# Performance work log

Hardware: AMD Instinct MI355X
Metric: run time of the kernel (lower is better)

## Reference

```python
import jax, jax.numpy as jnp
import numpy as np
from jax import lax

B, S, L = 128, 256, 10
WORD, CHAR = 50000, 100
TAGS, START, END = 32, 30, 31
WDIM, CDIM, FILT, H = 100, 30, 30, 100
LSTM_IN = WDIM + FILT  # 130
NEG = -10000.0


def setup_inputs() -> dict:
    key = jax.random.key(0)
    ks = jax.random.split(key, 24)
    sc = 0.1
    word_emb = (jax.random.normal(ks[0], (WORD, WDIM), jnp.float32) * sc).at[0].set(0.0)  # padding_idx=0
    char_emb = (jax.random.normal(ks[1], (CHAR, CDIM), jnp.float32) * sc).at[0].set(0.0)
    conv_w = jax.random.normal(ks[2], (FILT, 1, 3, CDIM), jnp.float32) * sc  # OIHW, kernel (3, char_dim)
    conv_b = jax.random.normal(ks[3], (FILT,), jnp.float32) * sc
    wih_f = jax.random.normal(ks[4], (4 * H, LSTM_IN), jnp.float32) * sc
    whh_f = jax.random.normal(ks[5], (4 * H, H), jnp.float32) * sc
    bih_f = jax.random.normal(ks[6], (4 * H,), jnp.float32) * sc
    bhh_f = jax.random.normal(ks[7], (4 * H,), jnp.float32) * sc
    wih_b = jax.random.normal(ks[8], (4 * H, LSTM_IN), jnp.float32) * sc
    whh_b = jax.random.normal(ks[9], (4 * H, H), jnp.float32) * sc
    bih_b = jax.random.normal(ks[10], (4 * H,), jnp.float32) * sc
    bhh_b = jax.random.normal(ks[11], (4 * H,), jnp.float32) * sc
    proj_w = jax.random.normal(ks[12], (TAGS, 2 * H), jnp.float32) * sc
    proj_b = jax.random.normal(ks[13], (TAGS,), jnp.float32) * sc
    trans = jax.random.normal(ks[14], (TAGS, TAGS), jnp.float32)
    trans = trans.at[:, START].set(NEG).at[END, :].set(NEG)  # CRF.reset_parm
    word_x = jax.random.randint(ks[15], (B, S), 1, WORD, jnp.int32)
    char_x = jax.random.randint(ks[16], (B, S, L), 1, CHAR, jnp.int32)
    y = jax.random.randint(ks[17], (B, S), 0, 30, jnp.int32)  # gold tags exclude start/end
    mask = jnp.ones((B, S), jnp.int32)
    return dict(word_emb=word_emb, char_emb=char_emb, conv_w=conv_w, conv_b=conv_b,
                wih_f=wih_f, whh_f=whh_f, bih_f=bih_f, bhh_f=bhh_f,
                wih_b=wih_b, whh_b=whh_b, bih_b=bih_b, bhh_b=bhh_b,
                proj_w=proj_w, proj_b=proj_b, trans=trans,
                word_x=word_x, char_x=char_x, y=y, mask=mask)


def _lstm_dir(x, wih, whh, bih, bhh, reverse):
    # x: [B, S, D] -> hidden states [B, S, H]; PyTorch gate order i, f, g, o
    b = bih + bhh
    xs = jnp.swapaxes(x, 0, 1)  # [S, B, D]
    if reverse:
        xs = xs[::-1]
    Bv = x.shape[0]
    Hd = whh.shape[1]
    init = (jnp.zeros((Bv, Hd), x.dtype), jnp.zeros((Bv, Hd), x.dtype))
    def step(carry, xt):
        h, c = carry
        g = xt @ wih.T + h @ whh.T + b  # [B, 4H]
        i, f, gg, o = jnp.split(g, 4, axis=-1)
        c = jax.nn.sigmoid(f) * c + jax.nn.sigmoid(i) * jnp.tanh(gg)
        h = jax.nn.sigmoid(o) * jnp.tanh(c)
        return (h, c), h
    _, hs = lax.scan(step, init, xs)
    if reverse:
        hs = hs[::-1]
    return jnp.swapaxes(hs, 0, 1)


def _forward(word_emb, char_emb, conv_w, conv_b, wih_f, whh_f, bih_f, bhh_f,
             wih_b, whh_b, bih_b, bhh_b, proj_w, proj_b, trans,
             word_x, char_x, y, mask):
    # --- CharCNN (dropout = identity in eval) ---
    ce = char_emb[char_x].reshape(B * S, 1, L, CDIM)  # [B*S, 1, L, CDIM]
    fm = lax.conv_general_dilated(ce, conv_w, (1, 1), ((2, 2), (0, 0)),
                                  dimension_numbers=('NCHW', 'OIHW', 'NCHW'))
    fm = fm + conv_b[None, :, None, None]  # [B*S, FILT, L+2, 1]
    char_feat = fm.max(axis=(2, 3)).reshape(B, S, FILT)
    # --- BiLSTM + projection ---
    x = jnp.concatenate([word_emb[word_x], char_feat], axis=-1)  # [B, S, 130]
    h_f = _lstm_dir(x, wih_f, whh_f, bih_f, bhh_f, False)
    h_b = _lstm_dir(x, wih_b, whh_b, bih_b, bhh_b, True)
    emission = jnp.concatenate([h_f, h_b], axis=-1) @ proj_w.T + proj_b  # [B, S, TAGS]
    maskf = mask.astype(emission.dtype)
    # --- CRF gold-path score (vectorized form of compute_y_score) ---
    y_pad = jnp.concatenate([jnp.full((B, 1), START, y.dtype), y], axis=1)  # [B, S+1]
    prev, cur = y_pad[:, :-1], y_pad[:, 1:]
    p = jnp.take_along_axis(emission, cur[..., None].astype(jnp.int32), axis=-1)[..., 0]
    t = trans[prev, cur]
    score_y = ((p + t) * maskf).sum(axis=1) + trans[y[:, -1], END]  # original uses last label unmasked
    # --- CRF partition function (logsumexp scan over time) ---
    la0 = jnp.full((B, TAGS), NEG, emission.dtype).at[:, START].set(0.0)
    def step(la, em_m):
        em, m = em_m  # em: [B, TAGS], m: [B]
        la2 = jax.nn.logsumexp(la[:, :, None] + trans[None, :, :] + em[:, None, :], axis=1)
        m = m[:, None]
        return la2 * m + la * (1.0 - m), None
    la, _ = lax.scan(step, la0, (jnp.swapaxes(emission, 0, 1), maskf.T))
    la = la + trans[:, END][None, :]
    total = jax.nn.logsumexp(la, axis=1, keepdims=True)  # [B, 1]
    # faithful to original: [B] - [B,1] broadcasts to [B,B], then mean
    return -jnp.mean(score_y - total)


def reference(word_emb, char_emb, conv_w, conv_b, wih_f, whh_f, bih_f, bhh_f,
              wih_b, whh_b, bih_b, bhh_b, proj_w, proj_b, trans,
              word_x, char_x, y, mask):
    return _forward(word_emb, char_emb, conv_w, conv_b, wih_f, whh_f, bih_f, bhh_f,
                    wih_b, whh_b, bih_b, bhh_b, proj_w, proj_b, trans,
                    word_x, char_x, y, mask)
```

## Files before the change

kernel.cpp:

```cpp
#include <hip/hip_runtime.h>
#include <hip/hip_fp16.h>
#include <cstdint>
#include <cstddef>

#define BB 128
#define SS 256
#define LL 10
#define NTAGS 32
#define TAG_START 30
#define TAG_END 31
#define WDIM 100
#define CDIM 30
#define NFILT 30
#define HDIM 100
#define KIN 130
#define KPAD 160
#define GDIM 400
#define NROWS 832
#define NEGV -10000.0f
#define CTOK 8

#define NB_CONV (BB * SS / CTOK)
#define NB_WORD (BB * SS * KPAD / 256)
#define NB_WCVT (NROWS * KPAD / 256)
#define NB_PRE  (NB_CONV + NB_WORD + NB_WCVT)

typedef _Float16 h2 __attribute__((ext_vector_type(2)));
typedef _Float16 f16x8 __attribute__((ext_vector_type(8)));
typedef float f32x4 __attribute__((ext_vector_type(4)));

__device__ __forceinline__ float sigm(float x) { return 1.0f / (1.0f + __expf(-x)); }
__device__ __forceinline__ float tanh_fast(float x) { return 2.0f / (1.0f + __expf(-2.0f * x)) - 1.0f; }

__device__ __forceinline__ void barrier_lds_only() {
  asm volatile("s_waitcnt lgkmcnt(0)" ::: "memory");
  __builtin_amdgcn_s_barrier();
  asm volatile("" ::: "memory");
}

__global__ __launch_bounds__(256) void k_pre(
    const float* __restrict__ wemb, const int* __restrict__ wx,
    const float* __restrict__ cemb, const float* __restrict__ convw,
    const float* __restrict__ convb, const int* __restrict__ cx,
    const float* __restrict__ wihF, const float* __restrict__ wihB,
    _Float16* __restrict__ x16, _Float16* __restrict__ w16,
    float* __restrict__ out) {
  int blk = blockIdx.x;
  int tid = threadIdx.x;
  if (blk == 0 && tid == 0) out[0] = 0.f;

  if (blk < NB_CONV) {
    int tok8 = tid >> 5;
    int f = tid & 31;
    int token0 = blk * CTOK;
    __shared__ float e[CTOK][LL * CDIM];
    __shared__ float cw[NFILT * 3 * CDIM];
    __shared__ float cb[NFILT];
    __shared__ int ci[CTOK][LL];
    if (tid < CTOK * LL) {
      int t = tid / LL, l = tid - t * LL;
      ci[t][l] = cx[(token0 + t) * LL + l];
    }
    for (int i = tid; i < NFILT * 3 * CDIM; i += 256) cw[i] = convw[i];
    if (tid < NFILT) cb[tid] = convb[tid];
    __syncthreads();
    for (int i = tid; i < CTOK * LL * CDIM; i += 256) {
      int t = i / (LL * CDIM);
      int r = i - t * (LL * CDIM);
      int l = r / CDIM, c = r - l * CDIM;
      e[t][l * CDIM + c] = cemb[ci[t][l] * CDIM + c];
    }
    __syncthreads();
    if (f < NFILT) {
      float d0[LL], d1[LL], d2[LL];
#pragma unroll
      for (int l = 0; l < LL; l++) { d0[l] = 0.f; d1[l] = 0.f; d2[l] = 0.f; }
      const float* et = &e[tok8][0];
      for (int c = 0; c < CDIM; c++) {
        float w0 = cw[(f * 3 + 0) * CDIM + c];
        float w1 = cw[(f * 3 + 1) * CDIM + c];
        float w2 = cw[(f * 3 + 2) * CDIM + c];
#pragma unroll
        for (int l = 0; l < LL; l++) {
          float ev = et[l * CDIM + c];
          d0[l] += ev * w0; d1[l] += ev * w1; d2[l] += ev * w2;
        }
      }
      float bias = cb[f];
      float m = -3.0e38f;
#pragma unroll
      for (int h = 0; h < LL + 2; h++) {
        float acc = bias;
        int j0 = h - 2, j1 = h - 1, j2 = h;
        if (j0 >= 0 && j0 < LL) acc += d0[j0];
        if (j1 >= 0 && j1 < LL) acc += d1[j1];
        if (j2 >= 0 && j2 < LL) acc += d2[j2];
        m = fmaxf(m, acc);
      }
      x16[(size_t)(token0 + tok8) * KPAD + WDIM + f] = (_Float16)m;
    }
  } else if (blk < NB_CONV + NB_WORD) {
    int idx = (blk - NB_CONV) * 256 + tid;
    int token = idx / KPAD;
    int d = idx - token * KPAD;
    if (d < WDIM) {
      x16[idx] = (_Float16)wemb[(size_t)wx[token] * WDIM + d];
    } else if (d >= KIN) {
      x16[idx] = (_Float16)0.f;
    }
  } else {
    int idx = (blk - NB_CONV - NB_WORD) * 256 + tid;
    int n = idx / KPAD;
    int k = idx - n * KPAD;
    float v = 0.f;
    if (k < KIN && n < 2 * GDIM) {
      v = (n < GDIM) ? wihF[(size_t)n * KIN + k] : wihB[(size_t)(n - GDIM) * KIN + k];
    }
    w16[idx] = (_Float16)v;
  }
}

__global__ __launch_bounds__(256) void k_pregemm(
    const _Float16* __restrict__ x16, const _Float16* __restrict__ w16,
    const float* __restrict__ bihF, const float* __restrict__ bhhF,
    const float* __restrict__ bihB, const float* __restrict__ bhhB,
    _Float16* __restrict__ preF, _Float16* __restrict__ preB) {
  __shared__ __align__(16) _Float16 Asl[64 * 40];
  __shared__ __align__(16) _Float16 Bsl[64 * 40];
  int m0 = blockIdx.x * 64;
  int n0 = blockIdx.y * 64;
  int tid = threadIdx.x;
  int lane = tid & 63, w = tid >> 6;
  int quad = lane >> 4, l15 = lane & 15;

  f32x4 acc[4];
#pragma unroll
  for (int i = 0; i < 4; i++) acc[i] = (f32x4){0.f, 0.f, 0.f, 0.f};

  int r = tid >> 2;
  int kk = (tid & 3) * 8;
  const _Float16* xs = x16 + (size_t)(m0 + r) * KPAD + kk;
  const _Float16* wsrc = w16 + (size_t)(n0 + r) * KPAD + kk;

  for (int kc = 0; kc < 5; kc++) {
    if (kc) __syncthreads();
    *(f16x8*)&Asl[r * 40 + kk] = *(const f16x8*)(xs + kc * 32);
    *(f16x8*)&Bsl[r * 40 + kk] = *(const f16x8*)(wsrc + kc * 32);
    __syncthreads();

    f16x8 bfrag = *(const f16x8*)&Bsl[(w * 16 + l15) * 40 + quad * 8];
#pragma unroll
    for (int mt = 0; mt < 4; mt++) {
      f16x8 afrag = *(const f16x8*)&Asl[(mt * 16 + l15) * 40 + quad * 8];
      acc[mt] = __builtin_amdgcn_mfma_f32_16x16x32_f16(afrag, bfrag, acc[mt], 0, 0, 0);
    }
  }

  int ng = n0 + w * 16 + l15;
  if (ng < 2 * GDIM) {
    int dir = ng >= GDIM;
    int jb = dir ? ng - GDIM : ng;
    _Float16* dst = dir ? preB : preF;
    float bias = (dir ? bihB : bihF)[jb] + (dir ? bhhB : bhhF)[jb];
#pragma unroll
    for (int mt = 0; mt < 4; mt++) {
#pragma unroll
      for (int i = 0; i < 4; i++) {
        int m = m0 + mt * 16 + quad * 4 + i;
        dst[(size_t)m * GDIM + jb] = (_Float16)(acc[mt][i] + bias);
      }
    }
  }
}

__global__ __launch_bounds__(448) void k_lstm(
    const _Float16* __restrict__ preF, const _Float16* __restrict__ preB,
    const float* __restrict__ whhF, const float* __restrict__ whhB,
    _Float16* __restrict__ hbuf) {
  int blk = blockIdx.x;
  int dir = blk >> 7;
  int b = blk & 127;
  const _Float16* pre = dir ? preB : preF;
  const float* whh = dir ? whhB : whhF;
  int tid = threadIdx.x;
  int kg = tid / 112;
  int rg = tid - kg * 112;
  bool act = (kg < 4) && (rg < 100);
  int r0 = act ? rg * 4 : 0;
  int kb = (act ? kg : 0) * 32;

  __half2 wp[4][8];
  {
#pragma unroll
    for (int i = 0; i < 4; i++) {
      const float* wr = whh + (size_t)(r0 + i) * HDIM;
#pragma unroll
      for (int q = 0; q < 8; q++) {
        int k0 = kb + 2 * q;
        float w0 = (k0 < HDIM) ? wr[k0] : 0.f;
        float w1 = (k0 + 1 < HDIM) ? wr[k0 + 1] : 0.f;
        wp[i][q] = __floats2half2_rn(w0, w1);
      }
    }
  }

  __shared__ __align__(16) _Float16 hsh16[2][128];
  __shared__ __align__(16) float gpart[4][GDIM];
  if (tid < 128) { hsh16[0][tid] = (_Float16)0.f; hsh16[1][tid] = (_Float16)0.f; }
  float c = 0.f;

  const _Float16* pbase = pre + ((size_t)b * SS + (dir ? (SS - 1) : 0)) * GDIM + r0;
  const intptr_t pstep = dir ? -(intptr_t)GDIM : (intptr_t)GDIM;
  uint2 p0 = {0, 0}, p1 = {0, 0};
  if (act && kg == 0) {
    p0 = *(const uint2*)pbase;
    p1 = *(const uint2*)(pbase + pstep);
  }
  __syncthreads();

  int cur = 0;
  for (int step = 0; step < SS; step++) {
    uint2 p2 = {0, 0};
    if (act && kg == 0) {
      int tn = (step + 2 < SS) ? (step + 2) : (SS - 1);
      p2 = *(const uint2*)(pbase + (intptr_t)tn * pstep);
    }

    if (act) {
      const uint4* h4 = (const uint4*)&hsh16[cur][kb];
      uint4 hv0 = h4[0], hv1 = h4[1];
      __half2 hp[8];
      hp[0] = __builtin_bit_cast(__half2, hv0.x);
      hp[1] = __builtin_bit_cast(__half2, hv0.y);
      hp[2] = __builtin_bit_cast(__half2, hv0.z);
      hp[3] = __builtin_bit_cast(__half2, hv0.w);
      hp[4] = __builtin_bit_cast(__half2, hv1.x);
      hp[5] = __builtin_bit_cast(__half2, hv1.y);
      hp[6] = __builtin_bit_cast(__half2, hv1.z);
      hp[7] = __builtin_bit_cast(__half2, hv1.w);

      float racc[4];
      __half2 z = __floats2half2_rn(0.f, 0.f);
#pragma unroll
      for (int i = 0; i < 4; i++) {
        __half2 a0 = z, a1 = z;
#pragma unroll
        for (int q = 0; q < 8; q += 2) {
          a0 = __hfma2(wp[i][q], hp[q], a0);
          a1 = __hfma2(wp[i][q + 1], hp[q + 1], a1);
        }
        racc[i] = (__low2float(a0) + __high2float(a0)) +
                  (__low2float(a1) + __high2float(a1));
      }
      if (kg == 0) {
        __half2 pa = __builtin_bit_cast(__half2, p0.x);
        __half2 pbv = __builtin_bit_cast(__half2, p0.y);
        racc[0] += __low2float(pa);
        racc[1] += __high2float(pa);
        racc[2] += __low2float(pbv);
        racc[3] += __high2float(pbv);
      }
      *(f32x4*)&gpart[kg][r0] = (f32x4){racc[0], racc[1], racc[2], racc[3]};
    }
    barrier_lds_only();
    if (tid < HDIM) {
      int j = tid;
      float gi = (gpart[0][j] + gpart[1][j]) + (gpart[2][j] + gpart[3][j]);
      float gf = (gpart[0][j + HDIM] + gpart[1][j + HDIM]) + (gpart[2][j + HDIM] + gpart[3][j + HDIM]);
      float gg = (gpart[0][j + 2 * HDIM] + gpart[1][j + 2 * HDIM]) + (gpart[2][j + 2 * HDIM] + gpart[3][j + 2 * HDIM]);
      float go = (gpart[0][j + 3 * HDIM] + gpart[1][j + 3 * HDIM]) + (gpart[2][j + 3 * HDIM] + gpart[3][j + 3 * HDIM]);
      float ig = sigm(gi), fg = sigm(gf), g2 = tanh_fast(gg), og = sigm(go);
      c = fg * c + ig * g2;
      float h = og * tanh_fast(c);
      hsh16[cur ^ 1][j] = (_Float16)h;
      int t = dir ? (SS - 1 - step) : step;
      hbuf[((size_t)b * SS + t) * (2 * HDIM) + dir * HDIM + j] = (_Float16)h;
    }
    barrier_lds_only();
    p0 = p1; p1 = p2;
    cur ^= 1;
  }
}

__global__ __launch_bounds__(256) void k_proj(const _Float16* __restrict__ hbuf,
                                              const float* __restrict__ pw,
                                              const float* __restrict__ pb,
                                              float* __restrict__ em) {
  __shared__ __align__(16) float pws[NTAGS * 204];
  __shared__ float pbs[NTAGS];
  int tid = threadIdx.x;
  for (int i = tid; i < NTAGS * 2 * HDIM; i += 256) {
    int tag = i / (2 * HDIM);
    int k = i - tag * (2 * HDIM);
    pws[tag * 204 + k] = pw[i];
  }
  if (tid < NTAGS) pbs[tid] = pb[tid];
  __syncthreads();

  int idx = blockIdx.x * blockDim.x + tid;
  if (idx >= BB * SS * NTAGS) return;
  int token = idx >> 5, tag = idx & 31;
  const uint4* h4 = (const uint4*)(hbuf + (size_t)token * 2 * HDIM);
  const float4* w4 = (const float4*)&pws[tag * 204];
  float acc = pbs[tag];
#pragma unroll
  for (int k = 0; k < 25; k++) {
    uint4 hv = h4[k];
    h2 a = __builtin_bit_cast(h2, hv.x);
    h2 bq = __builtin_bit_cast(h2, hv.y);
    h2 cq = __builtin_bit_cast(h2, hv.z);
    h2 d = __builtin_bit_cast(h2, hv.w);
    float4 w0 = w4[k * 2], w1 = w4[k * 2 + 1];
    acc += (float)a.x * w0.x + (float)a.y * w0.y + (float)bq.x * w0.z + (float)bq.y * w0.w
         + (float)cq.x * w1.x + (float)cq.y * w1.y + (float)d.x * w1.z + (float)d.y * w1.w;
  }
  em[idx] = acc;
}

__global__ __launch_bounds__(64) void k_crf(const float* __restrict__ em,
                                            const float* __restrict__ trans,
                                            const int* __restrict__ mask,
                                            const int* __restrict__ y,
                                            float* __restrict__ out) {
  int b = blockIdx.x;
  int lane = threadIdx.x;
  int j = lane & 31;
  int h = lane >> 5;

  float sacc = 0.f;
  for (int s = lane; s < SS; s += 64) {
    int curt = y[b * SS + s];
    int prevt = (s == 0) ? TAG_START : y[b * SS + s - 1];
    float mk = (float)mask[b * SS + s];
    sacc += (em[((size_t)b * SS + s) * NTAGS + curt] + trans[prevt * NTAGS + curt]) * mk;
  }
#pragma unroll
  for (int off = 32; off > 0; off >>= 1) sacc += __shfl_down(sacc, off);
  float scoreYv = __shfl(sacc, 0) + trans[y[b * SS + SS - 1] * NTAGS + TAG_END];

  float tcol[16];
#pragma unroll
  for (int i = 0; i < 16; i++) tcol[i] = trans[(h * 16 + i) * NTAGS + j];

  float la = (j == TAG_START) ? 0.f : NEGV;

  const float* emb = em + (size_t)b * SS * NTAGS + j;
  const int* mkb = mask + b * SS;
  float e0 = emb[0], e1 = emb[NTAGS];
  int m0i = mkb[0], m1i = mkb[1];

  for (int s = 0; s < SS; s++) {
    int sn = (s + 2 < SS) ? (s + 2) : (SS - 1);
    float e2 = emb[(size_t)sn * NTAGS];
    int m2i = mkb[sn];

    float v[16];
#pragma unroll
    for (int i = 0; i < 16; i++) v[i] = __shfl(la, h * 16 + i) + tcol[i];

    float ma = v[0], mb2 = v[1];
#pragma unroll
    for (int i = 2; i < 16; i += 2) { ma = fmaxf(ma, v[i]); mb2 = fmaxf(mb2, v[i + 1]); }
    float mh = fmaxf(ma, mb2);
    float m = fmaxf(mh, __shfl_xor(mh, 32));

    float sa = 0.f, sb = 0.f;
#pragma unroll
    for (int i = 0; i < 16; i += 2) { sa += __expf(v[i] - m); sb += __expf(v[i + 1] - m); }
    float sh = sa + sb;
    float sum = sh + __shfl_xor(sh, 32);

    float la2 = m + __logf(sum) + e0;
    float mk = (float)m0i;
    la = la2 * mk + la * (1.f - mk);
    e0 = e1; e1 = e2; m0i = m1i; m1i = m2i;
  }
  la += trans[j * NTAGS + TAG_END];

  float mm = la;
#pragma unroll
  for (int off = 16; off > 0; off >>= 1) mm = fmaxf(mm, __shfl_xor(mm, off));
  float ss = __expf(la - mm);
#pragma unroll
  for (int off = 16; off > 0; off >>= 1) ss += __shfl_xor(ss, off);
  float total = mm + __logf(ss);
  if (lane == 0) atomicAdd(out, (total - scoreYv) * (1.0f / BB));
}

extern "C" void kernel_launch(void* const* d_in, const int* in_sizes, int n_in,
                              void* d_out, int out_size, void* d_ws, size_t ws_size,
                              hipStream_t stream) {
  const float* word_emb = (const float*)d_in[0];
  const float* char_emb = (const float*)d_in[1];
  const float* conv_w   = (const float*)d_in[2];
  const float* conv_b   = (const float*)d_in[3];
  const float* wih_f    = (const float*)d_in[4];
  const float* whh_f    = (const float*)d_in[5];
  const float* bih_f    = (const float*)d_in[6];
  const float* bhh_f    = (const float*)d_in[7];
  const float* wih_b    = (const float*)d_in[8];
  const float* whh_b    = (const float*)d_in[9];
  const float* bih_b    = (const float*)d_in[10];
  const float* bhh_b    = (const float*)d_in[11];
  const float* proj_w   = (const float*)d_in[12];
  const float* proj_b   = (const float*)d_in[13];
  const float* trans    = (const float*)d_in[14];
  const int* word_x     = (const int*)d_in[15];
  const int* char_x     = (const int*)d_in[16];
  const int* y          = (const int*)d_in[17];
  const int* mask       = (const int*)d_in[18];
  float* out = (float*)d_out;

  _Float16* x16   = (_Float16*)d_ws;
  _Float16* w16   = x16 + (size_t)BB * SS * KPAD;
  _Float16* preF  = w16 + (size_t)NROWS * KPAD;
  _Float16* preB  = preF + (size_t)BB * SS * GDIM;
  _Float16* hbuf  = preB + (size_t)BB * SS * GDIM;
  float* em       = (float*)(hbuf + (size_t)BB * SS * 2 * HDIM);

  k_pre<<<NB_PRE, 256, 0, stream>>>(word_emb, word_x, char_emb, conv_w, conv_b,
                                    char_x, wih_f, wih_b, x16, w16, out);
  k_pregemm<<<dim3(BB * SS / 64, 13), 256, 0, stream>>>(x16, w16, bih_f, bhh_f,
                                                        bih_b, bhh_b, preF, preB);
  k_lstm<<<256, 448, 0, stream>>>(preF, preB, whh_f, whh_b, hbuf);
  k_proj<<<(BB * SS * NTAGS + 255) / 256, 256, 0, stream>>>(hbuf, proj_w, proj_b, em);
  k_crf<<<BB, 64, 0, stream>>>(em, trans, mask, y, out);
}
```

Before: 545.9 us.

## Batch 16 sequences per LSTM block and compute recurrence with MFMA

The LSTM kernel now handles 16 batch rows per block instead of one. The recurrent matvec becomes an MFMA 16x16x32 f16 GEMM, with the weight fragments held in registers and h stored in swizzled LDS. The pre-gate layout is transposed to [gate][time][batch] so each lane loads contiguous batch values, and one barrier per step replaces two. The launch shrinks from 256 to 16 blocks, which cuts per-step work overhead but leaves most CUs idle on a serial-latency-bound recurrence.

New measurement: 862.1 us. +57.9%, slower.

```diff
diff --git a/kernel.cpp b/kernel.cpp
--- a/kernel.cpp
+++ b/kernel.cpp
@@ -167,118 +167,128 @@
 #pragma unroll
       for (int i = 0; i < 4; i++) {
         int m = m0 + mt * 16 + quad * 4 + i;
-        dst[(size_t)m * GDIM + jb] = (_Float16)(acc[mt][i] + bias);
-      }
-    }
-  }
-}
-
+        dst[((size_t)jb * SS + (m & (SS - 1))) * BB + (m >> 8)] =
+            (_Float16)(acc[mt][i] + bias);
+      }
+    }
+  }
+}
+
+#define MB 16
 __global__ __launch_bounds__(448) void k_lstm(
     const _Float16* __restrict__ preF, const _Float16* __restrict__ preB,
     const float* __restrict__ whhF, const float* __restrict__ whhB,
     _Float16* __restrict__ hbuf) {
   int blk = blockIdx.x;
-  int dir = blk >> 7;
-  int b = blk & 127;
+  int dir = blk >> 3;
+  int b0 = (blk & 7) * MB;
   const _Float16* pre = dir ? preB : preF;
   const float* whh = dir ? whhB : whhF;
   int tid = threadIdx.x;
-  int kg = tid / 112;
-  int rg = tid - kg * 112;
-  bool act = (kg < 4) && (rg < 100);
-  int r0 = act ? rg * 4 : 0;
-  int kb = (act ? kg : 0) * 32;
-
-  __half2 wp[4][8];
-  {
-#pragma unroll
-    for (int i = 0; i < 4; i++) {
-      const float* wr = whh + (size_t)(r0 + i) * HDIM;
-#pragma unroll
-      for (int q = 0; q < 8; q++) {
-        int k0 = kb + 2 * q;
-        float w0 = (k0 < HDIM) ? wr[k0] : 0.f;
-        float w1 = (k0 + 1 < HDIM) ? wr[k0 + 1] : 0.f;
-        wp[i][q] = __floats2half2_rn(w0, w1);
-      }
-    }
-  }
-
-  __shared__ __align__(16) _Float16 hsh16[2][128];
-  __shared__ __align__(16) float gpart[4][GDIM];
-  if (tid < 128) { hsh16[0][tid] = (_Float16)0.f; hsh16[1][tid] = (_Float16)0.f; }
-  float c = 0.f;
-
-  const _Float16* pbase = pre + ((size_t)b * SS + (dir ? (SS - 1) : 0)) * GDIM + r0;
-  const intptr_t pstep = dir ? -(intptr_t)GDIM : (intptr_t)GDIM;
-  uint2 p0 = {0, 0}, p1 = {0, 0};
-  if (act && kg == 0) {
-    p0 = *(const uint2*)pbase;
-    p1 = *(const uint2*)(pbase + pstep);
-  }
+  int w = tid >> 6;
+  int lane = tid & 63;
+  int l15 = lane & 15, q = lane >> 4;
+  int j = w * 16 + l15;
+  bool jv = (j < HDIM);
+  int jc = jv ? j : 0;
+
+  f16x8 wfrag[4][4];
+#pragma unroll
+  for (int g = 0; g < 4; g++) {
+#pragma unroll
+    for (int kc = 0; kc < 4; kc++) {
+      float tmp[8] = {0.f, 0.f, 0.f, 0.f, 0.f, 0.f, 0.f, 0.f};
+      if (jv) {
+        const float* wr = whh + (size_t)(g * HDIM + j) * HDIM;
+#pragma unroll
+        for (int hh = 0; hh < 2; hh++) {
+          int kk = kc * 32 + q * 8 + hh * 4;
+          if (kk < HDIM) {
+            float4 v = *(const float4*)(wr + kk);
+            tmp[hh * 4 + 0] = v.x; tmp[hh * 4 + 1] = v.y;
+            tmp[hh * 4 + 2] = v.z; tmp[hh * 4 + 3] = v.w;
+          }
+        }
+      }
+      f16x8 fr;
+#pragma unroll
+      for (int e = 0; e < 8; e++) fr[e] = (_Float16)tmp[e];
+      wfrag[g][kc] = fr;
+    }
+  }
+
+  __shared__ __align__(16) _Float16 hA[2][MB * 128];
+  for (int idx = tid; idx < 2 * MB * 128; idx += 448) hA[0][idx] = (_Float16)0.f;
+
+  float cst[4] = {0.f, 0.f, 0.f, 0.f};
+
+  int t0 = dir ? (SS - 1) : 0;
+  const int tstep = dir ? -BB : BB;
+  const _Float16* pg[4];
+  uint2 p0[4], p1[4];
+#pragma unroll
+  for (int g = 0; g < 4; g++)
+    pg[g] = pre + ((size_t)(g * HDIM + jc) * SS + t0) * BB + b0 + q * 4;
   __syncthreads();
+#pragma unroll
+  for (int g = 0; g < 4; g++) { p0[g] = *(const uint2*)pg[g]; pg[g] += tstep; }
+#pragma unroll
+  for (int g = 0; g < 4; g++) { p1[g] = *(const uint2*)pg[g]; pg[g] += tstep; }
 
   int cur = 0;
-  for (int step = 0; step < SS; step++) {
-    uint2 p2 = {0, 0};
-    if (act && kg == 0) {
-      int tn = (step + 2 < SS) ? (step + 2) : (SS - 1);
-      p2 = *(const uint2*)(pbase + (intptr_t)tn * pstep);
-    }
-
-    if (act) {
-      const uint4* h4 = (const uint4*)&hsh16[cur][kb];
-      uint4 hv0 = h4[0], hv1 = h4[1];
-      __half2 hp[8];
-      hp[0] = __builtin_bit_cast(__half2, hv0.x);
-      hp[1] = __builtin_bit_cast(__half2, hv0.y);
-      hp[2] = __builtin_bit_cast(__half2, hv0.z);
-      hp[3] = __builtin_bit_cast(__half2, hv0.w);
-      hp[4] = __builtin_bit_cast(__half2, hv1.x);
-      hp[5] = __builtin_bit_cast(__half2, hv1.y);
-      hp[6] = __builtin_bit_cast(__half2, hv1.z);
-      hp[7] = __builtin_bit_cast(__half2, hv1.w);
-
-      float racc[4];
-      __half2 z = __floats2half2_rn(0.f, 0.f);
+  for (int step = 0; step <= SS; step++) {
+    if (step > 0 && tid < 400) {
+      int m = tid / 25, c4 = tid - m * 25;
+      int hidx = m * 128 + ((c4 * 4) ^ ((m & 7) << 3));
+      uint2 hv = *(const uint2*)&hA[cur][hidx];
+      int tprev = dir ? (SS - step) : (step - 1);
+      *(uint2*)&hbuf[((size_t)(b0 + m) * SS + tprev) * (2 * HDIM) + dir * HDIM + c4 * 4] = hv;
+    }
+    if (step == SS) break;
+
+    f16x8 af[4];
+#pragma unroll
+    for (int kc = 0; kc < 4; kc++) {
+      int off = kc * 32 + q * 8;
+      af[kc] = *(const f16x8*)&hA[cur][l15 * 128 + (off ^ ((l15 & 7) << 3))];
+    }
+
+    uint2 p2[4];
+#pragma unroll
+    for (int g = 0; g < 4; g++) { p2[g] = *(const uint2*)pg[g]; pg[g] += tstep; }
+
+    f32x4 acc[4];
+#pragma unroll
+    for (int g = 0; g < 4; g++) {
+      h2 lo = __builtin_bit_cast(h2, p0[g].x);
+      h2 hi = __builtin_bit_cast(h2, p0[g].y);
+      acc[g] = (f32x4){(float)lo.x, (float)lo.y, (float)hi.x, (float)hi.y};
+    }
+#pragma unroll
+    for (int kc = 0; kc < 4; kc++) {
+#pragma unroll
+      for (int g = 0; g < 4; g++) {
+        acc[g] = __builtin_amdgcn_mfma_f32_16x16x32_f16(af[kc], wfrag[g][kc], acc[g], 0, 0, 0);
+      }
+    }
+
+    int nbuf = cur ^ 1;
+    if (jv) {
 #pragma unroll
       for (int i = 0; i < 4; i++) {
-        __half2 a0 = z, a1 = z;
-#pragma unroll
-        for (int q = 0; q < 8; q += 2) {
-          a0 = __hfma2(wp[i][q], hp[q], a0);
-          a1 = __hfma2(wp[i][q + 1], hp[q + 1], a1);
-        }
-        racc[i] = (__low2float(a0) + __high2float(a0)) +
-                  (__low2float(a1) + __high2float(a1));
-      }
-      if (kg == 0) {
-        __half2 pa = __builtin_bit_cast(__half2, p0.x);
-        __half2 pbv = __builtin_bit_cast(__half2, p0.y);
-        racc[0] += __low2float(pa);
-        racc[1] += __high2float(pa);
-        racc[2] += __low2float(pbv);
-        racc[3] += __high2float(pbv);
-      }
-      *(f32x4*)&gpart[kg][r0] = (f32x4){racc[0], racc[1], racc[2], racc[3]};
-    }
+        float gi = acc[0][i], gf = acc[1][i], gg = acc[2][i], go = acc[3][i];
+        float ig = sigm(gi), fg = sigm(gf), g2 = tanh_fast(gg), og = sigm(go);
+        cst[i] = fg * cst[i] + ig * g2;
+        float h = og * tanh_fast(cst[i]);
+        int m = q * 4 + i;
+        hA[nbuf][m * 128 + (j ^ ((m & 7) << 3))] = (_Float16)h;
+      }
+    }
+
     barrier_lds_only();
-    if (tid < HDIM) {
-      int j = tid;
-      float gi = (gpart[0][j] + gpart[1][j]) + (gpart[2][j] + gpart[3][j]);
-      float gf = (gpart[0][j + HDIM] + gpart[1][j + HDIM]) + (gpart[2][j + HDIM] + gpart[3][j + HDIM]);
-      float gg = (gpart[0][j + 2 * HDIM] + gpart[1][j + 2 * HDIM]) + (gpart[2][j + 2 * HDIM] + gpart[3][j + 2 * HDIM]);
-      float go = (gpart[0][j + 3 * HDIM] + gpart[1][j + 3 * HDIM]) + (gpart[2][j + 3 * HDIM] + gpart[3][j + 3 * HDIM]);
-      float ig = sigm(gi), fg = sigm(gf), g2 = tanh_fast(gg), og = sigm(go);
-      c = fg * c + ig * g2;
-      float h = og * tanh_fast(c);
-      hsh16[cur ^ 1][j] = (_Float16)h;
-      int t = dir ? (SS - 1 - step) : step;
-      hbuf[((size_t)b * SS + t) * (2 * HDIM) + dir * HDIM + j] = (_Float16)h;
-    }
-    barrier_lds_only();
-    p0 = p1; p1 = p2;
     cur ^= 1;
+#pragma unroll
+    for (int g = 0; g < 4; g++) { p0[g] = p1[g]; p1[g] = p2[g]; }
   }
 }
 
@@ -422,7 +432,7 @@
                                     char_x, wih_f, wih_b, x16, w16, out);
   k_pregemm<<<dim3(BB * SS / 64, 13), 256, 0, stream>>>(x16, w16, bih_f, bhh_f,
                                                         bih_b, bhh_b, preF, preB);
-  k_lstm<<<256, 448, 0, stream>>>(preF, preB, whh_f, whh_b, hbuf);
+  k_lstm<<<16, 448, 0, stream>>>(preF, preB, whh_f, whh_b, hbuf);
   k_proj<<<(BB * SS * NTAGS + 255) / 256, 256, 0, stream>>>(hbuf, proj_w, proj_b, em);
   k_crf<<<BB, 64, 0, stream>>>(em, trans, mask, y, out);
 }
```

## Restructure LSTM recurrence so each thread pair owns one hidden unit's four gates

Applied to the files above, without the earlier changes.

The recurrent LSTM kernel is reorganized so each pair of threads computes all four gates for a single hidden unit, each covering half of the hidden dimension. The two halves are combined with a lane shuffle, which removes the LDS partial-gate buffer and one of the two per-step barriers. Block size drops from 448 to 256 threads. Each thread now keeps 100 half2 weights in registers, raising register pressure, and the per-timestep FMA chain becomes longer.

Result: no change. 537.4 us (-1.6%).

```diff
diff --git a/kernel.cpp b/kernel.cpp
--- a/kernel.cpp
+++ b/kernel.cpp
@@ -173,7 +173,7 @@
   }
 }
 
-__global__ __launch_bounds__(448) void k_lstm(
+__global__ __launch_bounds__(256, 1) void k_lstm(
     const _Float16* __restrict__ preF, const _Float16* __restrict__ preB,
     const float* __restrict__ whhF, const float* __restrict__ whhB,
     _Float16* __restrict__ hbuf) {
@@ -183,102 +183,106 @@
   const _Float16* pre = dir ? preB : preF;
   const float* whh = dir ? whhB : whhF;
   int tid = threadIdx.x;
-  int kg = tid / 112;
-  int rg = tid - kg * 112;
-  bool act = (kg < 4) && (rg < 100);
-  int r0 = act ? rg * 4 : 0;
-  int kb = (act ? kg : 0) * 32;
-
-  __half2 wp[4][8];
-  {
-#pragma unroll
-    for (int i = 0; i < 4; i++) {
-      const float* wr = whh + (size_t)(r0 + i) * HDIM;
-#pragma unroll
-      for (int q = 0; q < 8; q++) {
-        int k0 = kb + 2 * q;
-        float w0 = (k0 < HDIM) ? wr[k0] : 0.f;
-        float w1 = (k0 + 1 < HDIM) ? wr[k0 + 1] : 0.f;
-        wp[i][q] = __floats2half2_rn(w0, w1);
-      }
-    }
-  }
-
-  __shared__ __align__(16) _Float16 hsh16[2][128];
-  __shared__ __align__(16) float gpart[4][GDIM];
-  if (tid < 128) { hsh16[0][tid] = (_Float16)0.f; hsh16[1][tid] = (_Float16)0.f; }
+  int j = tid >> 1;
+  int kh = tid & 1;
+  bool act = (j < HDIM);
+  int jc = act ? j : 0;
+
+  __half2 wp[4][25];
+#pragma unroll
+  for (int g = 0; g < 4; g++) {
+    const float* wr = whh + (size_t)(g * HDIM + jc) * HDIM + kh * 50;
+#pragma unroll
+    for (int q = 0; q < 25; q++) {
+      wp[g][q] = __floats2half2_rn(wr[2 * q], wr[2 * q + 1]);
+    }
+  }
+
+  __shared__ __align__(16) _Float16 hsh[2][2][64];
+  if (tid < 128) ((int*)hsh)[tid] = 0;
   float c = 0.f;
 
-  const _Float16* pbase = pre + ((size_t)b * SS + (dir ? (SS - 1) : 0)) * GDIM + r0;
+  int t0 = dir ? (SS - 1) : 0;
   const intptr_t pstep = dir ? -(intptr_t)GDIM : (intptr_t)GDIM;
-  uint2 p0 = {0, 0}, p1 = {0, 0};
-  if (act && kg == 0) {
-    p0 = *(const uint2*)pbase;
-    p1 = *(const uint2*)(pbase + pstep);
-  }
+  const _Float16* pbase = pre + ((size_t)b * SS + t0) * GDIM + kh * 200 + jc;
+  _Float16 pa0 = pbase[0], pb0 = pbase[100];
+  _Float16 pa1 = pbase[pstep], pb1 = pbase[pstep + 100];
   __syncthreads();
 
   int cur = 0;
-  for (int step = 0; step < SS; step++) {
-    uint2 p2 = {0, 0};
-    if (act && kg == 0) {
-      int tn = (step + 2 < SS) ? (step + 2) : (SS - 1);
-      p2 = *(const uint2*)(pbase + (intptr_t)tn * pstep);
-    }
-
-    if (act) {
-      const uint4* h4 = (const uint4*)&hsh16[cur][kb];
-      uint4 hv0 = h4[0], hv1 = h4[1];
-      __half2 hp[8];
-      hp[0] = __builtin_bit_cast(__half2, hv0.x);
-      hp[1] = __builtin_bit_cast(__half2, hv0.y);
-      hp[2] = __builtin_bit_cast(__half2, hv0.z);
-      hp[3] = __builtin_bit_cast(__half2, hv0.w);
-      hp[4] = __builtin_bit_cast(__half2, hv1.x);
-      hp[5] = __builtin_bit_cast(__half2, hv1.y);
-      hp[6] = __builtin_bit_cast(__half2, hv1.z);
-      hp[7] = __builtin_bit_cast(__half2, hv1.w);
-
-      float racc[4];
-      __half2 z = __floats2half2_rn(0.f, 0.f);
-#pragma unroll
-      for (int i = 0; i < 4; i++) {
-        __half2 a0 = z, a1 = z;
-#pragma unroll
-        for (int q = 0; q < 8; q += 2) {
-          a0 = __hfma2(wp[i][q], hp[q], a0);
-          a1 = __hfma2(wp[i][q + 1], hp[q + 1], a1);
-        }
-        racc[i] = (__low2float(a0) + __high2float(a0)) +
-                  (__low2float(a1) + __high2float(a1));
-      }
-      if (kg == 0) {
-        __half2 pa = __builtin_bit_cast(__half2, p0.x);
-        __half2 pbv = __builtin_bit_cast(__half2, p0.y);
-        racc[0] += __low2float(pa);
-        racc[1] += __high2float(pa);
-        racc[2] += __low2float(pbv);
-        racc[3] += __high2float(pbv);
-      }
-      *(f32x4*)&gpart[kg][r0] = (f32x4){racc[0], racc[1], racc[2], racc[3]};
-    }
+  for (int s = 0; s < SS; s++) {
+    int sn = (s + 2 < SS) ? (s + 2) : (SS - 1);
+    const _Float16* pn = pbase + (intptr_t)sn * pstep;
+    _Float16 pa2 = pn[0], pb2 = pn[100];
+
+    const _Float16* hseg = &hsh[cur][kh][0];
+    uint4 hv0 = *(const uint4*)(hseg);
+    uint4 hv1 = *(const uint4*)(hseg + 8);
+    uint4 hv2 = *(const uint4*)(hseg + 16);
+    uint4 hv3 = *(const uint4*)(hseg + 24);
+    uint4 hv4 = *(const uint4*)(hseg + 32);
+    uint4 hv5 = *(const uint4*)(hseg + 40);
+    uint32_t hv6 = *(const uint32_t*)(hseg + 48);
+    __half2 hp[25];
+    hp[0]  = __builtin_bit_cast(__half2, hv0.x);
+    hp[1]  = __builtin_bit_cast(__half2, hv0.y);
+    hp[2]  = __builtin_bit_cast(__half2, hv0.z);
+    hp[3]  = __builtin_bit_cast(__half2, hv0.w);
+    hp[4]  = __builtin_bit_cast(__half2, hv1.x);
+    hp[5]  = __builtin_bit_cast(__half2, hv1.y);
+    hp[6]  = __builtin_bit_cast(__half2, hv1.z);
+    hp[7]  = __builtin_bit_cast(__half2, hv1.w);
+    hp[8]  = __builtin_bit_cast(__half2, hv2.x);
+    hp[9]  = __builtin_bit_cast(__half2, hv2.y);
+    hp[10] = __builtin_bit_cast(__half2, hv2.z);
+    hp[11] = __builtin_bit_cast(__half2, hv2.w);
+    hp[12] = __builtin_bit_cast(__half2, hv3.x);
+    hp[13] = __builtin_bit_cast(__half2, hv3.y);
+    hp[14] = __builtin_bit_cast(__half2, hv3.z);
+    hp[15] = __builtin_bit_cast(__half2, hv3.w);
+    hp[16] = __builtin_bit_cast(__half2, hv4.x);
+    hp[17] = __builtin_bit_cast(__half2, hv4.y);
+    hp[18] = __builtin_bit_cast(__half2, hv4.z);
+    hp[19] = __builtin_bit_cast(__half2, hv4.w);
+    hp[20] = __builtin_bit_cast(__half2, hv5.x);
+    hp[21] = __builtin_bit_cast(__half2, hv5.y);
+    hp[22] = __builtin_bit_cast(__half2, hv5.z);
+    hp[23] = __builtin_bit_cast(__half2, hv5.w);
+    hp[24] = __builtin_bit_cast(__half2, hv6);
+
+    float racc[4];
+    __half2 z = __floats2half2_rn(0.f, 0.f);
+#pragma unroll
+    for (int g = 0; g < 4; g++) {
+      __half2 a0 = z, a1 = z;
+#pragma unroll
+      for (int q = 0; q < 25; q += 2) a0 = __hfma2(wp[g][q], hp[q], a0);
+#pragma unroll
+      for (int q = 1; q < 25; q += 2) a1 = __hfma2(wp[g][q], hp[q], a1);
+      racc[g] = (__low2float(a0) + __high2float(a0)) +
+                (__low2float(a1) + __high2float(a1));
+    }
+
+    if (kh == 0) { racc[0] += (float)pa0; racc[1] += (float)pb0; }
+    else         { racc[2] += (float)pa0; racc[3] += (float)pb0; }
+#pragma unroll
+    for (int g = 0; g < 4; g++) racc[g] += __shfl_xor(racc[g], 1);
+
+    float ig = sigm(racc[0]), fg = sigm(racc[1]);
+    float g2 = tanh_fast(racc[2]), og = sigm(racc[3]);
+    c = fg * c + ig * g2;
+    float h = og * tanh_fast(c);
+
+    if (act && kh == 0) {
+      int seg = (j >= 50) ? 1 : 0;
+      hsh[cur ^ 1][seg][j - seg * 50] = (_Float16)h;
+      int t = dir ? (SS - 1 - s) : s;
+      hbuf[((size_t)b * SS + t) * (2 * HDIM) + dir * HDIM + j] = (_Float16)h;
+    }
+
     barrier_lds_only();
-    if (tid < HDIM) {
-      int j = tid;
-      float gi = (gpart[0][j] + gpart[1][j]) + (gpart[2][j] + gpart[3][j]);
-      float gf = (gpart[0][j + HDIM] + gpart[1][j + HDIM]) + (gpart[2][j + HDIM] + gpart[3][j + HDIM]);
-      float gg = (gpart[0][j + 2 * HDIM] + gpart[1][j + 2 * HDIM]) + (gpart[2][j + 2 * HDIM] + gpart[3][j + 2 * HDIM]);
-      float go = (gpart[0][j + 3 * HDIM] + gpart[1][j + 3 * HDIM]) + (gpart[2][j + 3 * HDIM] + gpart[3][j + 3 * HDIM]);
-      float ig = sigm(gi), fg = sigm(gf), g2 = tanh_fast(gg), og = sigm(go);
-      c = fg * c + ig * g2;
-      float h = og * tanh_fast(c);
-      hsh16[cur ^ 1][j] = (_Float16)h;
-      int t = dir ? (SS - 1 - step) : step;
-      hbuf[((size_t)b * SS + t) * (2 * HDIM) + dir * HDIM + j] = (_Float16)h;
-    }
-    barrier_lds_only();
-    p0 = p1; p1 = p2;
     cur ^= 1;
+    pa0 = pa1; pb0 = pb1; pa1 = pa2; pb1 = pb2;
   }
 }
 
@@ -422,7 +426,7 @@
                                     char_x, wih_f, wih_b, x16, w16, out);
   k_pregemm<<<dim3(BB * SS / 64, 13), 256, 0, stream>>>(x16, w16, bih_f, bhh_f,
                                                         bih_b, bhh_b, preF, preB);
-  k_lstm<<<256, 448, 0, stream>>>(preF, preB, whh_f, whh_b, hbuf);
+  k_lstm<<<256, 256, 0, stream>>>(preF, preB, whh_f, whh_b, hbuf);
   k_proj<<<(BB * SS * NTAGS + 255) / 256, 256, 0, stream>>>(hbuf, proj_w, proj_b, em);
   k_crf<<<BB, 64, 0, stream>>>(em, trans, mask, y, out);
 }
```
